# Optimization experiments

Hardware: AMD Instinct MI355X
Metric: run time of the kernel (lower is better)

Reference implementation:

```python
import jax, jax.numpy as jnp
import numpy as np

MAX_DEPTH = 7
DEPTH_SIZES = [4 ** d for d in range(1, MAX_DEPTH + 1)]  # nodes per depth
N_NODES = sum(DEPTH_SIZES)  # 21844
N_TIMES = 48
HIDDEN = 1024
ENC_DIM = 256
B, S = 128, 32


def setup_inputs() -> dict:
    key = jax.random.key(0)
    k = jax.random.split(key, 6)
    return {
        "prefix_embedding": jax.random.normal(k[0], (B, S, HIDDEN), dtype=jnp.float32),
        "emb_matrix": jax.random.normal(k[1], (N_NODES, ENC_DIM), dtype=jnp.float32) * 0.02,
        "W_key": jax.random.normal(k[2], (HIDDEN, ENC_DIM), dtype=jnp.float32) * (1.0 / np.sqrt(ENC_DIM)),
        "b_key": jax.random.normal(k[3], (HIDDEN,), dtype=jnp.float32) * 0.01,
        "W_time": jax.random.normal(k[4], (N_TIMES, HIDDEN), dtype=jnp.float32) * (1.0 / np.sqrt(HIDDEN)),
        "b_time": jax.random.normal(k[5], (N_TIMES,), dtype=jnp.float32) * 0.01,
    }


def reference(prefix_embedding, emb_matrix, W_key, b_key, W_time, b_time):
    # keys = embedding_to_key(make_embedding_matrix(...)): [N_NODES, HIDDEN]
    keys = emb_matrix @ W_key.T + b_key
    # bmm(prefix [B,S,H], keys^T): keys identical across batch -> shared einsum
    scores = jnp.einsum("bsh,nh->bsn", prefix_embedding, keys)  # [B,S,N_NODES]
    # multitask: per-depth gather of the contiguous node block + log_softmax
    locations = []
    off = 0
    for n in DEPTH_SIZES:
        locations.append(jax.nn.log_softmax(scores[..., off:off + n], axis=-1))
        off += n
    time = jax.nn.log_softmax(prefix_embedding @ W_time.T + b_time, axis=-1)  # [B,S,N_TIMES]
    return tuple(locations) + (time,)
```

## Files before the change

kernel.cpp:

```cpp
#include <hip/hip_runtime.h>

#define NNODES 21844
#define ENC 256
#define HID 1024
#define ROWS 4096
#define NTIMES 48

typedef __attribute__((ext_vector_type(8))) short bf16x8;
typedef __attribute__((ext_vector_type(8))) unsigned short u16x8;
typedef __attribute__((ext_vector_type(4))) float f32x4;

__device__ const int g_off[8] = {0, 4, 20, 84, 340, 1364, 5460, 21844};

__device__ inline unsigned short f2bf(float f) {
  unsigned int u = __float_as_uint(f);
  u += 0x7FFF + ((u >> 16) & 1);
  return (unsigned short)(u >> 16);
}

__device__ inline int depth_of(int c) {
  return (c >= 4) + (c >= 20) + (c >= 84) + (c >= 340) + (c >= 1364) + (c >= 5460);
}

__global__ __launch_bounds__(256) void prep(const float* __restrict__ prefix,
                                            const float* __restrict__ emb,
                                            const float* __restrict__ Wk,
                                            const float* __restrict__ Wt,
                                            unsigned short* __restrict__ Pb16,
                                            unsigned short* __restrict__ Eb,
                                            unsigned short* __restrict__ WkT,
                                            float* __restrict__ WtT,
                                            float* __restrict__ S) {
  int bid = blockIdx.x, tid = threadIdx.x;
  if (bid < 4096) {
    int i = bid * 256 + tid;
    float4 v = reinterpret_cast<const float4*>(prefix)[i];
    ushort4 o; o.x = f2bf(v.x); o.y = f2bf(v.y); o.z = f2bf(v.z); o.w = f2bf(v.w);
    reinterpret_cast<ushort4*>(Pb16)[i] = o;
  } else if (bid < 9557) {
    int i = (bid - 4096) * 256 + tid;
    float4 v = reinterpret_cast<const float4*>(emb)[i];
    ushort4 o; o.x = f2bf(v.x); o.y = f2bf(v.y); o.z = f2bf(v.z); o.w = f2bf(v.w);
    reinterpret_cast<ushort4*>(Eb)[i] = o;
  } else if (bid < 10581) {
    int i = (bid - 9557) * 256 + tid;
    int e = i >> 10, h = i & 1023;
    WkT[i] = f2bf(Wk[h * ENC + e]);
  } else if (bid < 10773) {
    int i = (bid - 10581) * 256 + tid;
    int k = i / NTIMES, c = i % NTIMES;
    WtT[i] = Wt[c * HID + k];
  } else {
    int i = (bid - 10773) * 256 + tid;
    reinterpret_cast<float4*>(S)[i] = float4{0.f, 0.f, 0.f, 0.f};
  }
}

__global__ __launch_bounds__(256) void p2_mfma(const unsigned short* __restrict__ Ab,
                                               const unsigned short* __restrict__ Bb,
                                               unsigned short* __restrict__ P2) {
  int lane = threadIdx.x & 63, w = threadIdx.x >> 6;
  int lr = lane & 15, lg = lane >> 4;
  int m0 = blockIdx.y * 64 + w * 16;
  int nb = blockIdx.x * 64;
  f32x4 acc[4];
#pragma unroll
  for (int n = 0; n < 4; ++n) acc[n] = f32x4{0.f, 0.f, 0.f, 0.f};
  const unsigned short* Ap = Ab + (long)(m0 + lr) * HID + lg * 8;
  for (int kk = 0; kk < 32; ++kk) {
    bf16x8 a = *reinterpret_cast<const bf16x8*>(Ap + kk * 32);
#pragma unroll
    for (int n = 0; n < 4; ++n) {
      bf16x8 b = *reinterpret_cast<const bf16x8*>(Bb + (long)(nb + n * 16 + lr) * HID + kk * 32 + lg * 8);
      acc[n] = __builtin_amdgcn_mfma_f32_16x16x32_bf16(a, b, acc[n], 0, 0, 0);
    }
  }
#pragma unroll
  for (int n = 0; n < 4; ++n)
#pragma unroll
    for (int j = 0; j < 4; ++j)
      P2[(m0 + lg * 4 + j) * ENC + nb + n * 16 + lr] = f2bf(acc[n][j]);
}

#define GEMM_TILE_BODY                                                                     \
  __shared__ unsigned short As[128 * 64];                                                  \
  __shared__ unsigned short Bs[128 * 64];                                                  \
  int tid = threadIdx.x;                                                                   \
  int lane = tid & 63, w = tid >> 6;                                                       \
  int lr = lane & 15, lg = lane >> 4;                                                      \
  int wr = w >> 1, wc = w & 1;                                                             \
  int m0 = blockIdx.x * 128, n0 = blockIdx.y * 128;                                        \
  int rr = tid >> 3, c8 = tid & 7;                                                         \
  f32x4 acc[4][4];                                                                         \
  _Pragma("unroll") for (int m = 0; m < 4; ++m)                                            \
    _Pragma("unroll") for (int n = 0; n < 4; ++n) acc[m][n] = f32x4{0.f, 0.f, 0.f, 0.f};   \
  for (int kt = 0; kt < 4; ++kt) {                                                         \
    if (kt) __syncthreads();                                                               \
    _Pragma("unroll") for (int r = 0; r < 4; ++r) {                                        \
      const unsigned short* ga = P2 + (long)(m0 + r * 32 + rr) * ENC + kt * 64 + c8 * 8;   \
      __builtin_amdgcn_global_load_lds(                                                    \
          (const __attribute__((address_space(1))) unsigned int*)ga,                       \
          (__attribute__((address_space(3))) unsigned int*)(As + r * 2048 + w * 512),      \
          16, 0, 0);                                                                       \
      int er = n0 + r * 32 + rr;                                                           \
      if (er > NNODES - 1) er = NNODES - 1;                                                \
      const unsigned short* gb = E + (long)er * ENC + kt * 64 + c8 * 8;                    \
      __builtin_amdgcn_global_load_lds(                                                    \
          (const __attribute__((address_space(1))) unsigned int*)gb,                       \
          (__attribute__((address_space(3))) unsigned int*)(Bs + r * 2048 + w * 512),      \
          16, 0, 0);                                                                       \
    }                                                                                      \
    __syncthreads();                                                                       \
    _Pragma("unroll") for (int kk = 0; kk < 2; ++kk) {                                     \
      bf16x8 a[4], b[4];                                                                   \
      _Pragma("unroll") for (int m = 0; m < 4; ++m)                                        \
        a[m] = *reinterpret_cast<const bf16x8*>(As + (wr * 64 + m * 16 + lr) * 64 + kk * 32 + lg * 8); \
      _Pragma("unroll") for (int n = 0; n < 4; ++n)                                        \
        b[n] = *reinterpret_cast<const bf16x8*>(Bs + (wc * 64 + n * 16 + lr) * 64 + kk * 32 + lg * 8); \
      _Pragma("unroll") for (int m = 0; m < 4; ++m)                                        \
        _Pragma("unroll") for (int n = 0; n < 4; ++n)                                      \
          acc[m][n] = __builtin_amdgcn_mfma_f32_16x16x32_bf16(a[m], b[n], acc[m][n], 0, 0, 0); \
    }                                                                                      \
  }

template <int BF16S>
__global__ __launch_bounds__(256) void gemm_stash(const unsigned short* __restrict__ P2,
                                                  const unsigned short* __restrict__ E,
                                                  unsigned short* __restrict__ stash,
                                                  float* __restrict__ outp,
                                                  float* __restrict__ S) {
  GEMM_TILE_BODY
  int rbase = m0 + wr * 64 + lg * 4;
  int hstart = n0 + wc * 64;
#pragma unroll
  for (int n = 0; n < 4; ++n) {
    int gc = hstart + n * 16 + lr;
    if (gc < NNODES) {
      int d = depth_of(gc);
      long ob = ((long)g_off[d] << 12) + (gc - g_off[d]);
      int sh = 2 * (d + 1);
#pragma unroll
      for (int m = 0; m < 4; ++m)
#pragma unroll
        for (int j = 0; j < 4; ++j) {
          int row = rbase + m * 16 + j;
          long idx = ob + ((long)row << sh);
          if (BF16S) stash[idx] = f2bf(acc[m][n][j]);
          else       outp[idx]  = acc[m][n][j];
        }
    }
  }
  int dlo = depth_of(hstart);
  int hend = hstart + 63; if (hend > NNODES - 1) hend = NNODES - 1;
  int dhi = depth_of(hend);
  int cd[4];
#pragma unroll
  for (int n = 0; n < 4; ++n) {
    int gc = hstart + n * 16 + lr;
    cd[n] = (gc < NNODES) ? depth_of(gc) : 99;
  }
#pragma unroll
  for (int m = 0; m < 4; ++m)
#pragma unroll
    for (int n = 0; n < 4; ++n)
#pragma unroll
      for (int j = 0; j < 4; ++j) acc[m][n][j] = __expf(acc[m][n][j]);
  for (int dt = dlo; dt <= dhi; ++dt) {
#pragma unroll
    for (int m = 0; m < 4; ++m) {
      float s[4] = {0.f, 0.f, 0.f, 0.f};
#pragma unroll
      for (int n = 0; n < 4; ++n) {
        bool use = (cd[n] == dt);
#pragma unroll
        for (int j = 0; j < 4; ++j) s[j] += use ? acc[m][n][j] : 0.f;
      }
#pragma unroll
      for (int j = 0; j < 4; ++j)
#pragma unroll
        for (int o = 1; o < 16; o <<= 1) s[j] += __shfl_xor(s[j], o);
      if (lr == 0) {
#pragma unroll
        for (int j = 0; j < 4; ++j)
          atomicAdd(&S[dt * ROWS + rbase + m * 16 + j], s[j]);
      }
    }
  }
}

template <int BF16S>
__global__ __launch_bounds__(256) void sub_write(const unsigned short* __restrict__ stash,
                                                 const float* __restrict__ S,
                                                 float* __restrict__ out) {
  long base = (long)blockIdx.x * 2048 + threadIdx.x * 8;
  int d = (base >= 16384) + (base >= 81920) + (base >= 344064) +
          (base >= 1392640) + (base >= 5586944) + (base >= 22364160);
  long bd = (d == 0) ? 0L : (d == 1) ? 16384L : (d == 2) ? 81920L : (d == 3) ? 344064L
          : (d == 4) ? 1392640L : (d == 5) ? 5586944L : 22364160L;
  long rel = base - bd;
  const float* sp = S + d * ROWS;
  float v[8];
  if (BF16S) {
    u16x8 u = *reinterpret_cast<const u16x8*>(stash + base);
#pragma unroll
    for (int j = 0; j < 8; ++j) v[j] = __uint_as_float((unsigned)(unsigned short)u[j] << 16);
  } else {
    float4 a = reinterpret_cast<const float4*>(out + base)[0];
    float4 b = reinterpret_cast<const float4*>(out + base)[1];
    v[0] = a.x; v[1] = a.y; v[2] = a.z; v[3] = a.w;
    v[4] = b.x; v[5] = b.y; v[6] = b.z; v[7] = b.w;
  }
  float4 o0, o1;
  if (d == 0) {
    int r0 = (int)(rel >> 2);
    float l0 = __logf(sp[r0]), l1 = __logf(sp[r0 + 1]);
    o0 = float4{v[0] - l0, v[1] - l0, v[2] - l0, v[3] - l0};
    o1 = float4{v[4] - l1, v[5] - l1, v[6] - l1, v[7] - l1};
  } else {
    int row = (int)(rel >> (2 * (d + 1)));
    float l = __logf(sp[row]);
    o0 = float4{v[0] - l, v[1] - l, v[2] - l, v[3] - l};
    o1 = float4{v[4] - l, v[5] - l, v[6] - l, v[7] - l};
  }
  reinterpret_cast<float4*>(out + base)[0] = o0;
  reinterpret_cast<float4*>(out + base)[1] = o1;
}

__global__ __launch_bounds__(256) void time_head(const float* __restrict__ prefix,
                                                 const float* __restrict__ WtT,
                                                 const float* __restrict__ bt,
                                                 float* __restrict__ out) {
  int lane = threadIdx.x & 63;
  int row = blockIdx.x * 4 + (threadIdx.x >> 6);
  const float4* pr = reinterpret_cast<const float4*>(prefix + (long)row * HID);
  float acc = -3.4e38f;
  if (lane < NTIMES) {
    float a = 0.f;
#pragma unroll 4
    for (int q = 0; q < HID / 4; ++q) {
      float4 pv = pr[q];
      const float* wrow = WtT + q * 4 * NTIMES;
      a += pv.x * wrow[lane] + pv.y * wrow[NTIMES + lane] +
           pv.z * wrow[2 * NTIMES + lane] + pv.w * wrow[3 * NTIMES + lane];
    }
    acc = a + bt[lane];
  }
  float m = acc;
#pragma unroll
  for (int d = 32; d; d >>= 1) m = fmaxf(m, __shfl_xor(m, d));
  float e = (lane < NTIMES) ? __expf(acc - m) : 0.f;
  float s = e;
#pragma unroll
  for (int d = 32; d; d >>= 1) s += __shfl_xor(s, d);
  if (lane < NTIMES) out[89473024 + row * NTIMES + lane] = acc - m - __logf(s);
}

extern "C" void kernel_launch(void* const* d_in, const int* in_sizes, int n_in,
                              void* d_out, int out_size, void* d_ws, size_t ws_size,
                              hipStream_t stream) {
  const float* prefix = (const float*)d_in[0];
  const float* emb    = (const float*)d_in[1];
  const float* Wk     = (const float*)d_in[2];
  const float* Wt     = (const float*)d_in[4];
  const float* bt     = (const float*)d_in[5];
  float* out = (float*)d_out;
  char* ws = (char*)d_ws;

  unsigned short* P2    = (unsigned short*)(ws + 0);
  unsigned short* Eb    = (unsigned short*)(ws + 2097152);
  unsigned short* WkT   = (unsigned short*)(ws + 13281280);
  unsigned short* Pb16  = (unsigned short*)(ws + 13805568);
  float*          WtT   = (float*)(ws + 22194176);
  float*          S     = (float*)(ws + 22390784);
  unsigned short* stash = (unsigned short*)(ws + 22505472);
  const size_t WS_NEED_STASH = 22505472UL + 178946048UL;

  bool big = ws_size >= WS_NEED_STASH;

  prep<<<10801, 256, 0, stream>>>(prefix, emb, Wk, Wt, Pb16, Eb, WkT, WtT, S);

  p2_mfma<<<dim3(4, 64), 256, 0, stream>>>(Pb16, WkT, P2);

  if (big) {
    gemm_stash<1><<<dim3(32, 171), 256, 0, stream>>>(P2, Eb, stash, out, S);
    sub_write<1><<<43688, 256, 0, stream>>>(stash, S, out);
  } else {
    gemm_stash<0><<<dim3(32, 171), 256, 0, stream>>>(P2, Eb, stash, out, S);
    sub_write<0><<<43688, 256, 0, stream>>>(stash, S, out);
  }

  time_head<<<1024, 256, 0, stream>>>(prefix, WtT, bt, out);
}
```

Measured before the change: 345.7 us.

## Double-buffer GEMM LDS staging, fold time head into sub_write, nontemporal stores

The main GEMM now uses two LDS buffers. The next K-slice is prefetched with global_load_lds while MFMAs run on the current one, so each k-step needs one barrier instead of two. The time-head kernel is merged into sub_write as extra trailing blocks, which removes one launch and lets it overlap the streaming writes. The output stores in sub_write and the time head become nontemporal to avoid cache pollution. Doubled LDS use (64KB per block) may lower occupancy of the GEMM.

```diff
diff --git a/kernel.cpp b/kernel.cpp
--- a/kernel.cpp
+++ b/kernel.cpp
@@ -82,54 +82,68 @@
       P2[(m0 + lg * 4 + j) * ENC + nb + n * 16 + lr] = f2bf(acc[n][j]);
 }
 
-#define GEMM_TILE_BODY                                                                     \
-  __shared__ unsigned short As[128 * 64];                                                  \
-  __shared__ unsigned short Bs[128 * 64];                                                  \
-  int tid = threadIdx.x;                                                                   \
-  int lane = tid & 63, w = tid >> 6;                                                       \
-  int lr = lane & 15, lg = lane >> 4;                                                      \
-  int wr = w >> 1, wc = w & 1;                                                             \
-  int m0 = blockIdx.x * 128, n0 = blockIdx.y * 128;                                        \
-  int rr = tid >> 3, c8 = tid & 7;                                                         \
-  f32x4 acc[4][4];                                                                         \
-  _Pragma("unroll") for (int m = 0; m < 4; ++m)                                            \
-    _Pragma("unroll") for (int n = 0; n < 4; ++n) acc[m][n] = f32x4{0.f, 0.f, 0.f, 0.f};   \
-  for (int kt = 0; kt < 4; ++kt) {                                                         \
-    if (kt) __syncthreads();                                                               \
-    _Pragma("unroll") for (int r = 0; r < 4; ++r) {                                        \
-      const unsigned short* ga = P2 + (long)(m0 + r * 32 + rr) * ENC + kt * 64 + c8 * 8;   \
-      __builtin_amdgcn_global_load_lds(                                                    \
-          (const __attribute__((address_space(1))) unsigned int*)ga,                       \
-          (__attribute__((address_space(3))) unsigned int*)(As + r * 2048 + w * 512),      \
-          16, 0, 0);                                                                       \
-      int er = n0 + r * 32 + rr;                                                           \
-      if (er > NNODES - 1) er = NNODES - 1;                                                \
-      const unsigned short* gb = E + (long)er * ENC + kt * 64 + c8 * 8;                    \
-      __builtin_amdgcn_global_load_lds(                                                    \
-          (const __attribute__((address_space(1))) unsigned int*)gb,                       \
-          (__attribute__((address_space(3))) unsigned int*)(Bs + r * 2048 + w * 512),      \
-          16, 0, 0);                                                                       \
-    }                                                                                      \
-    __syncthreads();                                                                       \
-    _Pragma("unroll") for (int kk = 0; kk < 2; ++kk) {                                     \
-      bf16x8 a[4], b[4];                                                                   \
-      _Pragma("unroll") for (int m = 0; m < 4; ++m)                                        \
-        a[m] = *reinterpret_cast<const bf16x8*>(As + (wr * 64 + m * 16 + lr) * 64 + kk * 32 + lg * 8); \
-      _Pragma("unroll") for (int n = 0; n < 4; ++n)                                        \
-        b[n] = *reinterpret_cast<const bf16x8*>(Bs + (wc * 64 + n * 16 + lr) * 64 + kk * 32 + lg * 8); \
-      _Pragma("unroll") for (int m = 0; m < 4; ++m)                                        \
-        _Pragma("unroll") for (int n = 0; n < 4; ++n)                                      \
-          acc[m][n] = __builtin_amdgcn_mfma_f32_16x16x32_bf16(a[m], b[n], acc[m][n], 0, 0, 0); \
-    }                                                                                      \
-  }
-
 template <int BF16S>
 __global__ __launch_bounds__(256) void gemm_stash(const unsigned short* __restrict__ P2,
                                                   const unsigned short* __restrict__ E,
                                                   unsigned short* __restrict__ stash,
                                                   float* __restrict__ outp,
                                                   float* __restrict__ S) {
-  GEMM_TILE_BODY
+  __shared__ unsigned short SH[2][2][128 * 64];
+  int tid = threadIdx.x;
+  int lane = tid & 63, w = tid >> 6;
+  int lr = lane & 15, lg = lane >> 4;
+  int wr = w >> 1, wc = w & 1;
+  int m0 = blockIdx.x * 128, n0 = blockIdx.y * 128;
+  int rr = tid >> 3, c8 = tid & 7;
+
+  f32x4 acc[4][4];
+#pragma unroll
+  for (int m = 0; m < 4; ++m)
+#pragma unroll
+    for (int n = 0; n < 4; ++n) acc[m][n] = f32x4{0.f, 0.f, 0.f, 0.f};
+
+#define STAGE(buf, kt)                                                                    \
+  _Pragma("unroll") for (int r = 0; r < 4; ++r) {                                         \
+    const unsigned short* ga = P2 + (long)(m0 + r * 32 + rr) * ENC + (kt) * 64 + c8 * 8;  \
+    __builtin_amdgcn_global_load_lds(                                                     \
+        (const __attribute__((address_space(1))) unsigned int*)ga,                        \
+        (__attribute__((address_space(3))) unsigned int*)(&SH[buf][0][r * 2048 + w * 512]), \
+        16, 0, 0);                                                                        \
+    int er = n0 + r * 32 + rr;                                                            \
+    if (er > NNODES - 1) er = NNODES - 1;                                                 \
+    const unsigned short* gb = E + (long)er * ENC + (kt) * 64 + c8 * 8;                   \
+    __builtin_amdgcn_global_load_lds(                                                     \
+        (const __attribute__((address_space(1))) unsigned int*)gb,                        \
+        (__attribute__((address_space(3))) unsigned int*)(&SH[buf][1][r * 2048 + w * 512]), \
+        16, 0, 0);                                                                        \
+  }
+
+  STAGE(0, 0)
+  __syncthreads();
+  for (int kt = 0; kt < 4; ++kt) {
+    int cur = kt & 1;
+    if (kt < 3) { STAGE(cur ^ 1, kt + 1) }
+    const unsigned short* As = &SH[cur][0][0];
+    const unsigned short* Bs = &SH[cur][1][0];
+#pragma unroll
+    for (int kk = 0; kk < 2; ++kk) {
+      bf16x8 a[4], b[4];
+#pragma unroll
+      for (int m = 0; m < 4; ++m)
+        a[m] = *reinterpret_cast<const bf16x8*>(As + (wr * 64 + m * 16 + lr) * 64 + kk * 32 + lg * 8);
+#pragma unroll
+      for (int n = 0; n < 4; ++n)
+        b[n] = *reinterpret_cast<const bf16x8*>(Bs + (wc * 64 + n * 16 + lr) * 64 + kk * 32 + lg * 8);
+#pragma unroll
+      for (int m = 0; m < 4; ++m)
+#pragma unroll
+        for (int n = 0; n < 4; ++n)
+          acc[m][n] = __builtin_amdgcn_mfma_f32_16x16x32_bf16(a[m], b[n], acc[m][n], 0, 0, 0);
+    }
+    __syncthreads();
+  }
+#undef STAGE
+
   int rbase = m0 + wr * 64 + lg * 4;
   int hstart = n0 + wc * 64;
 #pragma unroll
@@ -191,7 +205,37 @@
 template <int BF16S>
 __global__ __launch_bounds__(256) void sub_write(const unsigned short* __restrict__ stash,
                                                  const float* __restrict__ S,
-                                                 float* __restrict__ out) {
+                                                 float* __restrict__ out,
+                                                 const float* __restrict__ prefix,
+                                                 const float* __restrict__ WtT,
+                                                 const float* __restrict__ bt) {
+  if (blockIdx.x >= 43688) {
+    int lane = threadIdx.x & 63;
+    int row = (blockIdx.x - 43688) * 4 + (threadIdx.x >> 6);
+    const float4* pr = reinterpret_cast<const float4*>(prefix + (long)row * HID);
+    float acc = -3.4e38f;
+    if (lane < NTIMES) {
+      float a = 0.f;
+#pragma unroll 4
+      for (int q = 0; q < HID / 4; ++q) {
+        float4 pv = pr[q];
+        const float* wrow = WtT + q * 4 * NTIMES;
+        a += pv.x * wrow[lane] + pv.y * wrow[NTIMES + lane] +
+             pv.z * wrow[2 * NTIMES + lane] + pv.w * wrow[3 * NTIMES + lane];
+      }
+      acc = a + bt[lane];
+    }
+    float m = acc;
+#pragma unroll
+    for (int d = 32; d; d >>= 1) m = fmaxf(m, __shfl_xor(m, d));
+    float e = (lane < NTIMES) ? __expf(acc - m) : 0.f;
+    float s = e;
+#pragma unroll
+    for (int d = 32; d; d >>= 1) s += __shfl_xor(s, d);
+    if (lane < NTIMES)
+      __builtin_nontemporal_store(acc - m - __logf(s), out + 89473024 + row * NTIMES + lane);
+    return;
+  }
   long base = (long)blockIdx.x * 2048 + threadIdx.x * 8;
   int d = (base >= 16384) + (base >= 81920) + (base >= 344064) +
           (base >= 1392640) + (base >= 5586944) + (base >= 22364160);
@@ -210,49 +254,21 @@
     v[0] = a.x; v[1] = a.y; v[2] = a.z; v[3] = a.w;
     v[4] = b.x; v[5] = b.y; v[6] = b.z; v[7] = b.w;
   }
-  float4 o0, o1;
+  f32x4 o0, o1;
   if (d == 0) {
     int r0 = (int)(rel >> 2);
     float l0 = __logf(sp[r0]), l1 = __logf(sp[r0 + 1]);
-    o0 = float4{v[0] - l0, v[1] - l0, v[2] - l0, v[3] - l0};
-    o1 = float4{v[4] - l1, v[5] - l1, v[6] - l1, v[7] - l1};
+    o0 = f32x4{v[0] - l0, v[1] - l0, v[2] - l0, v[3] - l0};
+    o1 = f32x4{v[4] - l1, v[5] - l1, v[6] - l1, v[7] - l1};
   } else {
     int row = (int)(rel >> (2 * (d + 1)));
     float l = __logf(sp[row]);
-    o0 = float4{v[0] - l, v[1] - l, v[2] - l, v[3] - l};
-    o1 = float4{v[4] - l, v[5] - l, v[6] - l, v[7] - l};
-  }
-  reinterpret_cast<float4*>(out + base)[0] = o0;
-  reinterpret_cast<float4*>(out + base)[1] = o1;
-}
-
-__global__ __launch_bounds__(256) void time_head(const float* __restrict__ prefix,
-                                                 const float* __restrict__ WtT,
-                                                 const float* __restrict__ bt,
-                                                 float* __restrict__ out) {
-  int lane = threadIdx.x & 63;
-  int row = blockIdx.x * 4 + (threadIdx.x >> 6);
-  const float4* pr = reinterpret_cast<const float4*>(prefix + (long)row * HID);
-  float acc = -3.4e38f;
-  if (lane < NTIMES) {
-    float a = 0.f;
-#pragma unroll 4
-    for (int q = 0; q < HID / 4; ++q) {
-      float4 pv = pr[q];
-      const float* wrow = WtT + q * 4 * NTIMES;
-      a += pv.x * wrow[lane] + pv.y * wrow[NTIMES + lane] +
-           pv.z * wrow[2 * NTIMES + lane] + pv.w * wrow[3 * NTIMES + lane];
-    }
-    acc = a + bt[lane];
-  }
-  float m = acc;
-#pragma unroll
-  for (int d = 32; d; d >>= 1) m = fmaxf(m, __shfl_xor(m, d));
-  float e = (lane < NTIMES) ? __expf(acc - m) : 0.f;
-  float s = e;
-#pragma unroll
-  for (int d = 32; d; d >>= 1) s += __shfl_xor(s, d);
-  if (lane < NTIMES) out[89473024 + row * NTIMES + lane] = acc - m - __logf(s);
+    o0 = f32x4{v[0] - l, v[1] - l, v[2] - l, v[3] - l};
+    o1 = f32x4{v[4] - l, v[5] - l, v[6] - l, v[7] - l};
+  }
+  f32x4* op = reinterpret_cast<f32x4*>(out + base);
+  __builtin_nontemporal_store(o0, op);
+  __builtin_nontemporal_store(o1, op + 1);
 }
 
 extern "C" void kernel_launch(void* const* d_in, const int* in_sizes, int n_in,
@@ -283,11 +299,9 @@
 
   if (big) {
     gemm_stash<1><<<dim3(32, 171), 256, 0, stream>>>(P2, Eb, stash, out, S);
-    sub_write<1><<<43688, 256, 0, stream>>>(stash, S, out);
+    sub_write<1><<<44712, 256, 0, stream>>>(stash, S, out, prefix, WtT, bt);
   } else {
     gemm_stash<0><<<dim3(32, 171), 256, 0, stream>>>(P2, Eb, stash, out, S);
-    sub_write<0><<<43688, 256, 0, stream>>>(stash, S, out);
-  }
-
-  time_head<<<1024, 256, 0, stream>>>(prefix, WtT, bt, out);
-}
+    sub_write<0><<<44712, 256, 0, stream>>>(stash, S, out, prefix, WtT, bt);
+  }
+}
```

Measured after the change: 362.7 us. 1.05x slower.
